# Kernel optimization log

Hardware: AMD Instinct MI355X
Metric: run time of the kernel (lower is better)

The kernel has to match this reference:

```python
import math
import jax, jax.numpy as jnp
import numpy as np

B, N, C, H = 64, 197, 768, 12
KEEP_RATE = 0.7

def setup_inputs() -> dict:
    key = jax.random.key(0)
    k0, k1, k2 = jax.random.split(key, 3)
    x = jax.random.normal(k0, (B, N, C), jnp.float32)
    qkv_w = jax.random.normal(k1, (C, 3 * C), jnp.float32) * 0.02
    qkv_b = jnp.zeros((3 * C,), jnp.float32)
    proj_w = jax.random.normal(k2, (C, C), jnp.float32) * 0.02
    proj_b = jnp.zeros((C,), jnp.float32)
    return {"x": x, "qkv_w": qkv_w, "qkv_b": qkv_b, "proj_w": proj_w, "proj_b": proj_b}

def reference(x, qkv_w, qkv_b, proj_w, proj_b):
    b, n, c = x.shape
    d = c // H
    scale = d ** -0.5
    # qkv: [B,N,3C] -> [3,B,H,N,d]
    qkv = (x @ qkv_w + qkv_b).reshape(b, n, 3, H, d)
    qkv = jnp.transpose(qkv, (2, 0, 3, 1, 4))
    q, k, v = qkv[0], qkv[1], qkv[2]
    attn = jax.nn.softmax(jnp.einsum('bhnd,bhmd->bhnm', q, k) * scale, axis=-1)  # [B,H,N,N]
    out = jnp.einsum('bhnm,bhmd->bhnd', attn, v)          # [B,H,N,d]
    out = jnp.transpose(out, (0, 2, 1, 3)).reshape(b, n, c)
    x_out = out @ proj_w + proj_b                          # [B,N,C]
    # dynamic token pruning via CLS attention (row 0, excluding CLS itself)
    left_tokens = math.ceil(KEEP_RATE * (n - 1))
    cls_attn = attn[:, :, 0, 1:].mean(axis=1)              # [B,N-1]
    _, idx = jax.lax.top_k(cls_attn, left_tokens)          # descending, sorted
    index = jnp.broadcast_to(idx[:, :, None], (b, left_tokens, c))
    return (x_out, index, idx, cls_attn, left_tokens)
```

## Files before the change

### kernel.cpp

```cpp
#include <hip/hip_runtime.h>
#include <math.h>

#define BB   64
#define NTOK 197
#define CC   768
#define HH   12
#define DH   64
#define MTOT (BB * NTOK)
#define MPAD 12672
#define LEFT 138

#define XOUT_OFF  0
#define INDEX_OFF 9682944
#define IDX_OFF   16465920
#define CLS_OFF   16474752
#define LT_OFF    16487296

typedef short s8v __attribute__((ext_vector_type(8)));
typedef short s4v __attribute__((ext_vector_type(4)));
typedef float f4v __attribute__((ext_vector_type(4)));

#define GLOAD16(g, l) __builtin_amdgcn_global_load_lds( \
    (const __attribute__((address_space(1))) unsigned int*)(g), \
    (__attribute__((address_space(3))) unsigned int*)(l), 16, 0, 0)

__device__ __forceinline__ unsigned short f2bf(float f) {
    union { float f; unsigned int i; } x; x.f = f;
    unsigned int r = x.i + 0x7FFFu + ((x.i >> 16) & 1u);
    return (unsigned short)(r >> 16);
}

__global__ __launch_bounds__(256)
void convert_x(const float* __restrict__ in, unsigned short* __restrict__ outb)
{
    size_t i = ((size_t)blockIdx.x * 256 + threadIdx.x) * 8;
    float4 a = *(const float4*)(in + i);
    float4 b = *(const float4*)(in + i + 4);
    s8v r;
    r[0] = (short)f2bf(a.x); r[1] = (short)f2bf(a.y);
    r[2] = (short)f2bf(a.z); r[3] = (short)f2bf(a.w);
    r[4] = (short)f2bf(b.x); r[5] = (short)f2bf(b.y);
    r[6] = (short)f2bf(b.z); r[7] = (short)f2bf(b.w);
    *(s8v*)(outb + i) = r;
}

__global__ __launch_bounds__(256)
void transpose_w(const float* __restrict__ in, unsigned short* __restrict__ outb, int N)
{
    __shared__ float tile[32][33];
    const int bi = blockIdx.x, bj = blockIdx.y;
    const int tx = threadIdx.x & 31, ty = threadIdx.x >> 5;
#pragma unroll
    for (int r = ty; r < 32; r += 8)
        tile[r][tx] = in[(size_t)(bi * 32 + r) * N + bj * 32 + tx];
    __syncthreads();
#pragma unroll
    for (int r = ty; r < 32; r += 8)
        outb[(size_t)(bj * 32 + r) * 768 + bi * 32 + tx] = f2bf(tile[tx][r]);
}

__global__ __launch_bounds__(256)
void gemm_bf16(const unsigned short* __restrict__ A, const unsigned short* __restrict__ BT,
               const float* __restrict__ bias, int ncolt, int mode,
               unsigned short* __restrict__ outb, float* __restrict__ outf)
{
    const int id = blockIdx.x;
    const int xcd = id & 7;
    const int t = id >> 3;
    const int ct = t % ncolt, s = t / ncolt;
    const int rt = s * 8 + xcd;
    if (rt >= 99) return;
    const int m0 = rt * 128, n0 = ct * 128;

    const int tid = threadIdx.x;
    const int wave = tid >> 6, lane = tid & 63;
    const int quad = lane >> 4, l16 = lane & 15;
    const int rowbase = (wave >> 1) * 64, colbase = (wave & 1) * 64;
    __shared__ __align__(16) short As[128 * 64];
    __shared__ __align__(16) short Bs[128 * 64];

    const int rA   = lane >> 3;
    const int gcol = ((lane & 7) ^ rA) * 8;
    const unsigned short* gA[4];
    const unsigned short* gB[4];
#pragma unroll
    for (int i = 0; i < 4; ++i) {
        int c = wave * 4 + i;
        gA[i] = A  + (size_t)(m0 + c * 8 + rA) * 768 + gcol;
        gB[i] = BT + (size_t)(n0 + c * 8 + rA) * 768 + gcol;
    }
    int aoff[4], boff[4];
#pragma unroll
    for (int i = 0; i < 4; ++i) {
        aoff[i] = (rowbase + i * 16 + l16) * 64 + ((quad ^ (l16 & 7)) * 8);
        boff[i] = (colbase + i * 16 + l16) * 64 + ((quad ^ (l16 & 7)) * 8);
    }

    f4v acc[4][4];
#pragma unroll
    for (int i = 0; i < 4; ++i)
#pragma unroll
        for (int j = 0; j < 4; ++j) acc[i][j] = (f4v)0.f;

    for (int k0 = 0; k0 < 768; k0 += 64) {
#pragma unroll
        for (int i = 0; i < 4; ++i) {
            int c = wave * 4 + i;
            GLOAD16(gA[i] + k0, &As[c * 512]);
            GLOAD16(gB[i] + k0, &Bs[c * 512]);
        }
        __syncthreads();
#pragma unroll
        for (int ks = 0; ks < 2; ++ks) {
            const int x = ks * 32;
            s8v af[4], bf[4];
#pragma unroll
            for (int i = 0; i < 4; ++i) af[i] = *(const s8v*)&As[aoff[i] ^ x];
#pragma unroll
            for (int j = 0; j < 4; ++j) bf[j] = *(const s8v*)&Bs[boff[j] ^ x];
#pragma unroll
            for (int i = 0; i < 4; ++i)
#pragma unroll
                for (int j = 0; j < 4; ++j)
                    acc[i][j] = __builtin_amdgcn_mfma_f32_16x16x32_bf16(bf[j], af[i], acc[i][j], 0, 0, 0);
        }
        __syncthreads();
    }

    const int ncols = mode ? 768 : 2304;
#pragma unroll
    for (int i = 0; i < 4; ++i) {
        const int m = m0 + rowbase + i * 16 + l16;
        if (m >= MTOT) continue;
#pragma unroll
        for (int j = 0; j < 4; ++j) {
            const int nb = n0 + colbase + j * 16 + quad * 4;
            float4 b4 = *(const float4*)&bias[nb];
            if (mode == 1) {
                float4 r;
                r.x = acc[i][j][0] + b4.x; r.y = acc[i][j][1] + b4.y;
                r.z = acc[i][j][2] + b4.z; r.w = acc[i][j][3] + b4.w;
                *(float4*)(outf + (size_t)m * ncols + nb) = r;
            } else {
                s4v r;
                r[0] = (short)f2bf(acc[i][j][0] + b4.x);
                r[1] = (short)f2bf(acc[i][j][1] + b4.y);
                r[2] = (short)f2bf(acc[i][j][2] + b4.z);
                r[3] = (short)f2bf(acc[i][j][3] + b4.w);
                *(s4v*)(outb + (size_t)m * ncols + nb) = r;
            }
        }
    }
}

#define PSTR 228

__global__ __launch_bounds__(256)
void attn_mfma(const unsigned short* __restrict__ qkv, unsigned short* __restrict__ attnbf)
{
    const int bh = blockIdx.x;
    const int b = bh / HH, h = bh - b * HH;
    const int tid = threadIdx.x;
    const int wave = tid >> 6, lane = tid & 63;
    const int quad = lane >> 4, l16 = lane & 15;
    __shared__ short Vs[64 * PSTR];
    __shared__ short Ps[4][16 * PSTR];

    const unsigned short* qg = qkv + (size_t)b * NTOK * 2304 + h * DH;
    const unsigned short* kg = qg + 768;
    const unsigned short* vg = qg + 1536;

    if (tid < NTOK) {
#pragma unroll
        for (int c = 0; c < 8; ++c) {
            s8v vv = *(const s8v*)(vg + (size_t)tid * 2304 + c * 8);
#pragma unroll
            for (int e = 0; e < 8; ++e) Vs[(c * 8 + e) * PSTR + tid] = vv[e];
        }
    }
    for (int f = tid; f < 64 * (PSTR - NTOK); f += 256) {
        int dd = f / (PSTR - NTOK);
        int tk = NTOK + (f - dd * (PSTR - NTOK));
        Vs[dd * PSTR + tk] = 0;
    }
    __syncthreads();

    for (int strip = wave; strip < 13; strip += 4) {
        const int mq = min(strip * 16 + l16, NTOK - 1);
        const s8v aq0 = *(const s8v*)(qg + (size_t)mq * 2304 + quad * 8);
        const s8v aq1 = *(const s8v*)(qg + (size_t)mq * 2304 + 32 + quad * 8);

        f4v sacc[14];
#pragma unroll
        for (int j = 0; j < 14; ++j) sacc[j] = (f4v)0.f;
#pragma unroll
        for (int j = 0; j < 14; ++j) {
            const int kt = min(j * 16 + l16, NTOK - 1);
            s8v bk0 = *(const s8v*)(kg + (size_t)kt * 2304 + quad * 8);
            s8v bk1 = *(const s8v*)(kg + (size_t)kt * 2304 + 32 + quad * 8);
            sacc[j] = __builtin_amdgcn_mfma_f32_16x16x32_bf16(bk0, aq0, sacc[j], 0, 0, 0);
            sacc[j] = __builtin_amdgcn_mfma_f32_16x16x32_bf16(bk1, aq1, sacc[j], 0, 0, 0);
        }

        float mx = -1e30f;
#pragma unroll
        for (int j = 0; j < 14; ++j)
#pragma unroll
            for (int r = 0; r < 4; ++r) {
                const int key = j * 16 + quad * 4 + r;
                float s = (key < NTOK) ? sacc[j][r] * 0.125f : -1e30f;
                sacc[j][r] = s;
                mx = fmaxf(mx, s);
            }
        mx = fmaxf(mx, __shfl_xor(mx, 16, 64));
        mx = fmaxf(mx, __shfl_xor(mx, 32, 64));

        float sm = 0.f;
#pragma unroll
        for (int j = 0; j < 14; ++j) {
            s4v pk;
#pragma unroll
            for (int r = 0; r < 4; ++r) {
                const int key = j * 16 + quad * 4 + r;
                float p = (key < NTOK) ? __expf(sacc[j][r] - mx) : 0.f;
                sm += p;
                pk[r] = (short)f2bf(p);
            }
            *(s4v*)&Ps[wave][l16 * PSTR + j * 16 + quad * 4] = pk;
        }
        sm += __shfl_xor(sm, 16, 64);
        sm += __shfl_xor(sm, 32, 64);
        const float rcp = 1.f / sm;

        f4v oacc[4];
#pragma unroll
        for (int j = 0; j < 4; ++j) oacc[j] = (f4v)0.f;
#pragma unroll
        for (int t = 0; t < 7; ++t) {
            const int ko = t * 32 + quad * 8;
            s8v ap = *(const s8v*)&Ps[wave][l16 * PSTR + ko];
#pragma unroll
            for (int j = 0; j < 4; ++j) {
                s8v bv = *(const s8v*)&Vs[(j * 16 + l16) * PSTR + ko];
                oacc[j] = __builtin_amdgcn_mfma_f32_16x16x32_bf16(bv, ap, oacc[j], 0, 0, 0);
            }
        }
        const int qrow = strip * 16 + l16;
        if (qrow < NTOK) {
#pragma unroll
            for (int j = 0; j < 4; ++j) {
                s4v o4;
#pragma unroll
                for (int r = 0; r < 4; ++r) o4[r] = (short)f2bf(oacc[j][r] * rcp);
                *(s4v*)&attnbf[((size_t)b * NTOK + qrow) * 768 + h * DH + j * 16 + quad * 4] = o4;
            }
        }
    }
}

__global__ __launch_bounds__(256)
void qr_kernel(const float* __restrict__ x, const float* __restrict__ qkv_w,
               const float* __restrict__ qkv_b, float* __restrict__ rws,
               float* __restrict__ bconst)
{
    const int blk = blockIdx.x;
    const int b = blk / HH, h = blk - b * HH;
    const int tid = threadIdx.x;
    __shared__ float x0[CC];
    __shared__ float q0h[DH];
    for (int c = tid; c < CC; c += 256) x0[c] = x[(size_t)b * NTOK * CC + c];
    __syncthreads();
    if (tid < DH) {
        const int o = h * DH + tid;
        float acc = qkv_b[o];
        for (int c = 0; c < CC; ++c)
            acc = fmaf(x0[c], qkv_w[(size_t)c * 2304 + o], acc);
        q0h[tid] = acc;
    }
    __syncthreads();
    for (int c = tid; c < CC; c += 256) {
        const float* wrow = qkv_w + (size_t)c * 2304 + CC + h * DH;
        float acc = 0.f;
#pragma unroll
        for (int d = 0; d < DH; d += 4) {
            float4 w4 = *(const float4*)(wrow + d);
            acc = fmaf(w4.x, q0h[d + 0], acc);
            acc = fmaf(w4.y, q0h[d + 1], acc);
            acc = fmaf(w4.z, q0h[d + 2], acc);
            acc = fmaf(w4.w, q0h[d + 3], acc);
        }
        rws[((size_t)b * HH + h) * CC + c] = acc;
    }
    if (tid == 0) {
        float acc = 0.f;
        for (int d = 0; d < DH; ++d) acc += q0h[d] * qkv_b[CC + h * DH + d];
        bconst[blk] = acc;
    }
}

__global__ __launch_bounds__(256)
void cls_s(const float* __restrict__ x, const float* __restrict__ rws,
           const float* __restrict__ bconst, float* __restrict__ sws)
{
    const int id = blockIdx.x;
    const int b = id & 63, h = id >> 6;
    const int tid = threadIdx.x;
    __shared__ __align__(16) float rl[CC];
    __shared__ float bcs;
    for (int c = tid; c < CC; c += 256) rl[c] = rws[((size_t)b * HH + h) * CC + c];
    if (tid == 0) bcs = bconst[b * HH + h];
    __syncthreads();
    if (tid < NTOK) {
        const float* xr = x + ((size_t)b * NTOK + tid) * CC;
        float acc = 0.f;
        for (int c = 0; c < CC; c += 4) {
            float4 r4 = *(const float4*)&rl[c];
            float4 x4 = *(const float4*)(xr + c);
            acc = fmaf(x4.x, r4.x, acc);
            acc = fmaf(x4.y, r4.y, acc);
            acc = fmaf(x4.z, r4.z, acc);
            acc = fmaf(x4.w, r4.w, acc);
        }
        sws[((size_t)b * HH + h) * NTOK + tid] = (acc + bcs) * 0.125f;
    }
}

__global__ __launch_bounds__(256)
void cls_topk(const float* __restrict__ sws, float* __restrict__ out, int write_lt)
{
    const int b = blockIdx.x, tid = threadIdx.x;
    const int wave = tid >> 6, lane = tid & 63;
    __shared__ float sbuf[HH][208];
    __shared__ float pm[4][208];
    __shared__ float vals[256];
    __shared__ int   idxs[256];

    for (int jj = lane; jj < 208; jj += 64) pm[wave][jj] = 0.f;
    if (tid < NTOK) {
#pragma unroll
        for (int h = 0; h < HH; ++h)
            sbuf[h][tid] = sws[((size_t)b * HH + h) * NTOK + tid];
    }
    __syncthreads();

    for (int h = wave; h < HH; h += 4) {
        float sv[4], ev[4];
        float mx = -1e30f;
#pragma unroll
        for (int t = 0; t < 4; ++t) {
            int j = lane + 64 * t;
            sv[t] = (j < NTOK) ? sbuf[h][j] : -1e30f;
            mx = fmaxf(mx, sv[t]);
        }
#pragma unroll
        for (int off = 1; off < 64; off <<= 1) mx = fmaxf(mx, __shfl_xor(mx, off, 64));
        float sm = 0.f;
#pragma unroll
        for (int t = 0; t < 4; ++t) {
            int j = lane + 64 * t;
            ev[t] = (j < NTOK) ? expf(sv[t] - mx) : 0.f;
            sm += ev[t];
        }
#pragma unroll
        for (int off = 1; off < 64; off <<= 1) sm += __shfl_xor(sm, off, 64);
#pragma unroll
        for (int t = 0; t < 4; ++t) {
            int j = lane + 64 * t;
            if (j < NTOK) pm[wave][j] += ev[t] / sm;
        }
    }
    __syncthreads();

    float v = -INFINITY;
    int id = 256 + tid;
    if (tid < NTOK - 1) {
        int j = tid + 1;
        float s = ((pm[0][j] + pm[1][j]) + (pm[2][j] + pm[3][j])) * (1.f / 12.f);
        v = s; id = tid;
        out[CLS_OFF + (size_t)b * (NTOK - 1) + tid] = s;
    }
    vals[tid] = v; idxs[tid] = id;
    __syncthreads();

    for (int k = 2; k <= 256; k <<= 1) {
        for (int j = k >> 1; j > 0; j >>= 1) {
            int ixj = tid ^ j;
            if (ixj > tid) {
                float va = vals[tid], vb2 = vals[ixj];
                int ia = idxs[tid], ib = idxs[ixj];
                bool aLess = (va > vb2) || (va == vb2 && ia < ib);
                bool dir = ((tid & k) == 0);
                if (dir != aLess) {
                    vals[tid] = vb2; vals[ixj] = va;
                    idxs[tid] = ib;  idxs[ixj] = ia;
                }
            }
            __syncthreads();
        }
    }

    if (tid < LEFT) out[IDX_OFF + (size_t)b * LEFT + tid] = (float)idxs[tid];
    for (int u = tid; u < LEFT * CC; u += 256) {
        int t = u / CC;
        out[INDEX_OFF + (size_t)b * LEFT * CC + u] = (float)idxs[t];
    }
    if (write_lt && b == 0 && tid == 0) out[LT_OFF] = (float)LEFT;
}

extern "C" void kernel_launch(void* const* d_in, const int* in_sizes, int n_in,
                              void* d_out, int out_size, void* d_ws, size_t ws_size,
                              hipStream_t stream)
{
    const float* x      = (const float*)d_in[0];
    const float* qkv_w  = (const float*)d_in[1];
    const float* qkv_b  = (const float*)d_in[2];
    const float* proj_w = (const float*)d_in[3];
    const float* proj_b = (const float*)d_in[4];
    float* out = (float*)d_out;

    char* w = (char*)d_ws;
    unsigned short* xbf   = (unsigned short*)w; w += (size_t)MPAD * CC * 2;
    unsigned short* wt1   = (unsigned short*)w; w += (size_t)3 * CC * CC * 2;
    unsigned short* wt2   = (unsigned short*)w; w += (size_t)CC * CC * 2;
    unsigned short* qkvbf = (unsigned short*)w; w += (size_t)MTOT * 3 * CC * 2;
    unsigned short* atbf  = (unsigned short*)w; w += (size_t)MPAD * CC * 2;
    float* rws    = (float*)w; w += (size_t)BB * HH * CC * 4;
    float* bconst = (float*)w; w += (size_t)BB * HH * 4;
    float* sws    = (float*)w; w += (size_t)BB * HH * NTOK * 4;

    convert_x<<<dim3(4728), 256, 0, stream>>>(x, xbf);
    transpose_w<<<dim3(24, 72), 256, 0, stream>>>(qkv_w, wt1, 3 * CC);
    transpose_w<<<dim3(24, 24), 256, 0, stream>>>(proj_w, wt2, CC);
    gemm_bf16<<<dim3(8 * 18 * 13), 256, 0, stream>>>(xbf, wt1, qkv_b, 18, 0, qkvbf, nullptr);
    attn_mfma<<<dim3(BB * HH), 256, 0, stream>>>(qkvbf, atbf);
    gemm_bf16<<<dim3(8 * 6 * 13), 256, 0, stream>>>(atbf, wt2, proj_b, 6, 1,
                                                    nullptr, out + XOUT_OFF);
    qr_kernel<<<dim3(BB * HH), 256, 0, stream>>>(x, qkv_w, qkv_b, rws, bconst);
    cls_s<<<dim3(BB * HH), 256, 0, stream>>>(x, rws, bconst, sws);
    cls_topk<<<dim3(BB), 256, 0, stream>>>(sws, out, (out_size > LT_OFF) ? 1 : 0);
}
```

Before: 388.1 us.

## Double-buffer GEMM LDS tiles and merge prep and CLS-score kernels

```diff
diff --git a/kernel.cpp b/kernel.cpp
--- a/kernel.cpp
+++ b/kernel.cpp
@@ -31,24 +31,34 @@
 }
 
 __global__ __launch_bounds__(256)
-void convert_x(const float* __restrict__ in, unsigned short* __restrict__ outb)
-{
-    size_t i = ((size_t)blockIdx.x * 256 + threadIdx.x) * 8;
-    float4 a = *(const float4*)(in + i);
-    float4 b = *(const float4*)(in + i + 4);
-    s8v r;
-    r[0] = (short)f2bf(a.x); r[1] = (short)f2bf(a.y);
-    r[2] = (short)f2bf(a.z); r[3] = (short)f2bf(a.w);
-    r[4] = (short)f2bf(b.x); r[5] = (short)f2bf(b.y);
-    r[6] = (short)f2bf(b.z); r[7] = (short)f2bf(b.w);
-    *(s8v*)(outb + i) = r;
-}
-
-__global__ __launch_bounds__(256)
-void transpose_w(const float* __restrict__ in, unsigned short* __restrict__ outb, int N)
-{
+void prep(const float* __restrict__ x, const float* __restrict__ qkv_w,
+          const float* __restrict__ proj_w, unsigned short* __restrict__ xbf,
+          unsigned short* __restrict__ wt1, unsigned short* __restrict__ wt2)
+{
+    const int id = blockIdx.x;
+    if (id < 4728) {
+        size_t i = ((size_t)id * 256 + threadIdx.x) * 8;
+        float4 a = *(const float4*)(x + i);
+        float4 b = *(const float4*)(x + i + 4);
+        s8v r;
+        r[0] = (short)f2bf(a.x); r[1] = (short)f2bf(a.y);
+        r[2] = (short)f2bf(a.z); r[3] = (short)f2bf(a.w);
+        r[4] = (short)f2bf(b.x); r[5] = (short)f2bf(b.y);
+        r[6] = (short)f2bf(b.z); r[7] = (short)f2bf(b.w);
+        *(s8v*)(xbf + i) = r;
+        return;
+    }
     __shared__ float tile[32][33];
-    const int bi = blockIdx.x, bj = blockIdx.y;
+    const float* in;
+    unsigned short* outt;
+    int N, bi, bj;
+    if (id < 6456) {
+        int t = id - 4728; in = qkv_w; outt = wt1; N = 2304;
+        bi = t % 24; bj = t / 24;
+    } else {
+        int t = id - 6456; in = proj_w; outt = wt2; N = 768;
+        bi = t % 24; bj = t / 24;
+    }
     const int tx = threadIdx.x & 31, ty = threadIdx.x >> 5;
 #pragma unroll
     for (int r = ty; r < 32; r += 8)
@@ -56,7 +66,7 @@
     __syncthreads();
 #pragma unroll
     for (int r = ty; r < 32; r += 8)
-        outb[(size_t)(bj * 32 + r) * 768 + bi * 32 + tx] = f2bf(tile[tx][r]);
+        outt[(size_t)(bj * 32 + r) * 768 + bi * 32 + tx] = f2bf(tile[tx][r]);
 }
 
 __global__ __launch_bounds__(256)
@@ -76,18 +86,20 @@
     const int wave = tid >> 6, lane = tid & 63;
     const int quad = lane >> 4, l16 = lane & 15;
     const int rowbase = (wave >> 1) * 64, colbase = (wave & 1) * 64;
-    __shared__ __align__(16) short As[128 * 64];
-    __shared__ __align__(16) short Bs[128 * 64];
+    __shared__ __align__(16) short As[2 * 8192];
+    __shared__ __align__(16) short Bs[2 * 8192];
 
     const int rA   = lane >> 3;
     const int gcol = ((lane & 7) ^ rA) * 8;
     const unsigned short* gA[4];
     const unsigned short* gB[4];
+    int ldsoff[4];
 #pragma unroll
     for (int i = 0; i < 4; ++i) {
         int c = wave * 4 + i;
         gA[i] = A  + (size_t)(m0 + c * 8 + rA) * 768 + gcol;
         gB[i] = BT + (size_t)(n0 + c * 8 + rA) * 768 + gcol;
+        ldsoff[i] = c * 512;
     }
     int aoff[4], boff[4];
 #pragma unroll
@@ -102,29 +114,39 @@
 #pragma unroll
         for (int j = 0; j < 4; ++j) acc[i][j] = (f4v)0.f;
 
-    for (int k0 = 0; k0 < 768; k0 += 64) {
-#pragma unroll
-        for (int i = 0; i < 4; ++i) {
-            int c = wave * 4 + i;
-            GLOAD16(gA[i] + k0, &As[c * 512]);
-            GLOAD16(gB[i] + k0, &Bs[c * 512]);
-        }
+#pragma unroll
+    for (int i = 0; i < 4; ++i) {
+        GLOAD16(gA[i], &As[ldsoff[i]]);
+        GLOAD16(gB[i], &Bs[ldsoff[i]]);
+    }
+
+    for (int it = 0; it < 12; ++it) {
         __syncthreads();
+        if (it < 11) {
+            const int k0 = (it + 1) * 64;
+            const int bo = ((it + 1) & 1) * 8192;
+#pragma unroll
+            for (int i = 0; i < 4; ++i) {
+                GLOAD16(gA[i] + k0, &As[bo + ldsoff[i]]);
+                GLOAD16(gB[i] + k0, &Bs[bo + ldsoff[i]]);
+            }
+        }
+        const short* curA = &As[(it & 1) * 8192];
+        const short* curB = &Bs[(it & 1) * 8192];
 #pragma unroll
         for (int ks = 0; ks < 2; ++ks) {
             const int x = ks * 32;
             s8v af[4], bf[4];
 #pragma unroll
-            for (int i = 0; i < 4; ++i) af[i] = *(const s8v*)&As[aoff[i] ^ x];
-#pragma unroll
-            for (int j = 0; j < 4; ++j) bf[j] = *(const s8v*)&Bs[boff[j] ^ x];
+            for (int i = 0; i < 4; ++i) af[i] = *(const s8v*)&curA[aoff[i] ^ x];
+#pragma unroll
+            for (int j = 0; j < 4; ++j) bf[j] = *(const s8v*)&curB[boff[j] ^ x];
 #pragma unroll
             for (int i = 0; i < 4; ++i)
 #pragma unroll
                 for (int j = 0; j < 4; ++j)
                     acc[i][j] = __builtin_amdgcn_mfma_f32_16x16x32_bf16(bf[j], af[i], acc[i][j], 0, 0, 0);
         }
-        __syncthreads();
     }
 
     const int ncols = mode ? 768 : 2304;
@@ -259,15 +281,17 @@
 }
 
 __global__ __launch_bounds__(256)
-void qr_kernel(const float* __restrict__ x, const float* __restrict__ qkv_w,
-               const float* __restrict__ qkv_b, float* __restrict__ rws,
-               float* __restrict__ bconst)
-{
-    const int blk = blockIdx.x;
-    const int b = blk / HH, h = blk - b * HH;
+void qr_s(const float* __restrict__ x, const float* __restrict__ qkv_w,
+          const float* __restrict__ qkv_b, float* __restrict__ sws)
+{
+    const int id = blockIdx.x;
+    const int b = id & 63, h = id >> 6;
     const int tid = threadIdx.x;
     __shared__ float x0[CC];
     __shared__ float q0h[DH];
+    __shared__ __align__(16) float rl[CC];
+    __shared__ float bcs;
+
     for (int c = tid; c < CC; c += 256) x0[c] = x[(size_t)b * NTOK * CC + c];
     __syncthreads();
     if (tid < DH) {
@@ -289,26 +313,13 @@
             acc = fmaf(w4.z, q0h[d + 2], acc);
             acc = fmaf(w4.w, q0h[d + 3], acc);
         }
-        rws[((size_t)b * HH + h) * CC + c] = acc;
+        rl[c] = acc;
     }
     if (tid == 0) {
         float acc = 0.f;
         for (int d = 0; d < DH; ++d) acc += q0h[d] * qkv_b[CC + h * DH + d];
-        bconst[blk] = acc;
-    }
-}
-
-__global__ __launch_bounds__(256)
-void cls_s(const float* __restrict__ x, const float* __restrict__ rws,
-           const float* __restrict__ bconst, float* __restrict__ sws)
-{
-    const int id = blockIdx.x;
-    const int b = id & 63, h = id >> 6;
-    const int tid = threadIdx.x;
-    __shared__ __align__(16) float rl[CC];
-    __shared__ float bcs;
-    for (int c = tid; c < CC; c += 256) rl[c] = rws[((size_t)b * HH + h) * CC + c];
-    if (tid == 0) bcs = bconst[b * HH + h];
+        bcs = acc;
+    }
     __syncthreads();
     if (tid < NTOK) {
         const float* xr = x + ((size_t)b * NTOK + tid) * CC;
@@ -424,18 +435,13 @@
     unsigned short* wt2   = (unsigned short*)w; w += (size_t)CC * CC * 2;
     unsigned short* qkvbf = (unsigned short*)w; w += (size_t)MTOT * 3 * CC * 2;
     unsigned short* atbf  = (unsigned short*)w; w += (size_t)MPAD * CC * 2;
-    float* rws    = (float*)w; w += (size_t)BB * HH * CC * 4;
-    float* bconst = (float*)w; w += (size_t)BB * HH * 4;
     float* sws    = (float*)w; w += (size_t)BB * HH * NTOK * 4;
 
-    convert_x<<<dim3(4728), 256, 0, stream>>>(x, xbf);
-    transpose_w<<<dim3(24, 72), 256, 0, stream>>>(qkv_w, wt1, 3 * CC);
-    transpose_w<<<dim3(24, 24), 256, 0, stream>>>(proj_w, wt2, CC);
+    prep<<<dim3(7032), 256, 0, stream>>>(x, qkv_w, proj_w, xbf, wt1, wt2);
     gemm_bf16<<<dim3(8 * 18 * 13), 256, 0, stream>>>(xbf, wt1, qkv_b, 18, 0, qkvbf, nullptr);
     attn_mfma<<<dim3(BB * HH), 256, 0, stream>>>(qkvbf, atbf);
     gemm_bf16<<<dim3(8 * 6 * 13), 256, 0, stream>>>(atbf, wt2, proj_b, 6, 1,
                                                     nullptr, out + XOUT_OFF);
-    qr_kernel<<<dim3(BB * HH), 256, 0, stream>>>(x, qkv_w, qkv_b, rws, bconst);
-    cls_s<<<dim3(BB * HH), 256, 0, stream>>>(x, rws, bconst, sws);
+    qr_s<<<dim3(BB * HH), 256, 0, stream>>>(x, qkv_w, qkv_b, sws);
     cls_topk<<<dim3(BB), 256, 0, stream>>>(sws, out, (out_size > LT_OFF) ? 1 : 0);
 }
```

New measurement: 394.7 us. Within noise of the previous version (+1.7%).
